# Optimization experiments

Measured on AMD Instinct MI355X. Metric: run time of the kernel, lower is better.

The kernel has to match this reference:

```python
import jax, jax.numpy as jnp
import numpy as np

B, S, VOCAB, HID, NCLS = 64, 512, 1400, 256, 128


def _time_lstm(W_all, b_all, U_all, b_u, W_d, b_d, x, ts):
    # x: [b, s, h], ts: [b, s]
    b = x.shape[0]
    h0 = jnp.zeros((b, HID), x.dtype)
    c0 = jnp.zeros((b, HID), x.dtype)

    def step(carry, xt):
        h, c = carry
        x_t, t_t = xt  # [b,h], [b]
        c_s1 = jnp.tanh(c @ W_d.T + b_d)
        c_adj = (c - c_s1) + c_s1 * t_t[:, None]
        gates = jax.nn.sigmoid(h @ W_all.T + b_all + x_t @ U_all.T + b_u)
        f, i, o, c_tmp = jnp.split(gates, 4, axis=1)  # note: c_tmp is sigmoid, as in source
        c_new = f * c_adj + i * c_tmp
        h_new = o * jnp.tanh(c_new)
        return (h_new, c_new), h_new

    _, hs = jax.lax.scan(step, (h0, c0), (x.transpose(1, 0, 2), ts.T))
    return hs.transpose(1, 0, 2)  # [b, s, h]


def setup_inputs() -> dict:
    key = jax.random.key(0)
    ks = jax.random.split(key, 18)

    def g(k, shape, scale=0.05):
        return jax.random.normal(k, shape, dtype=jnp.float32) * scale

    return {
        "inputs": jax.random.uniform(ks[0], (B, S, VOCAB), dtype=jnp.float32),
        "timestamps": jax.random.uniform(ks[1], (B, S), dtype=jnp.float32),
        "emb": g(ks[2], (VOCAB, HID)),
        "W_all1": g(ks[3], (4 * HID, HID)), "b_all1": g(ks[4], (4 * HID,)),
        "U_all1": g(ks[5], (4 * HID, HID)), "b_u1": g(ks[6], (4 * HID,)),
        "W_d1": g(ks[7], (HID, HID)), "b_d1": g(ks[8], (HID,)),
        "W_all2": g(ks[9], (4 * HID, HID)), "b_all2": g(ks[10], (4 * HID,)),
        "U_all2": g(ks[11], (4 * HID, HID)), "b_u2": g(ks[12], (4 * HID,)),
        "W_d2": g(ks[13], (HID, HID)), "b_d2": g(ks[14], (HID,)),
        "wa": g(ks[15], (1, HID)),
        "Wb": g(ks[16], (HID, HID)),
        "W_out": g(ks[17], (NCLS, HID)),
    }


def reference(inputs, timestamps, emb, W_all1, b_all1, U_all1, b_u1, W_d1, b_d1,
              W_all2, b_all2, U_all2, b_u2, W_d2, b_d2, wa, Wb, W_out):
    embedded = jnp.einsum('bsv,vh->bsh', inputs, emb)  # multi-hot embedding lookup
    out1 = _time_lstm(W_all1, b_all1, U_all1, b_u1, W_d1, b_d1, embedded, timestamps)
    out2 = _time_lstm(W_all2, b_all2, U_all2, b_u2, W_d2, b_d2, embedded, timestamps)
    alpha = jax.nn.softmax(jnp.einsum('bsh,oh->bs', out1, wa), axis=1)  # [b,s]
    Beta = jnp.tanh(jnp.einsum('bsh,gh->bsg', out2, Wb))  # [b,s,h]
    ctx = jnp.sum(embedded * Beta * alpha[:, :, None], axis=1)  # [b,h]
    return ctx @ W_out.T  # [b, num_classes]
```

## Files before the change

kernel.cpp:

```cpp
#include <hip/hip_runtime.h>

typedef __attribute__((ext_vector_type(8))) short short8;
typedef __attribute__((ext_vector_type(4))) float f32x4;

#define B_   64
#define S_   512
#define V_   1400
#define VP_  1408
#define H_   256
#define G4_  1024
#define NC_  128
#define CH_  64

__device__ __forceinline__ unsigned short f2bf(float f) {
    unsigned u = __builtin_bit_cast(unsigned, f);
    u += 0x7FFFu + ((u >> 16) & 1u);
    return (unsigned short)(u >> 16);
}
__device__ __forceinline__ float bf2f(unsigned short h) {
    unsigned u = ((unsigned)h) << 16;
    return __builtin_bit_cast(float, u);
}
__device__ __forceinline__ float fsig(float x) {
    x = fminf(fmaxf(x, -40.f), 40.f);
    float e = __builtin_amdgcn_exp2f(x * -1.44269504f);
    return __builtin_amdgcn_rcpf(1.0f + e);
}
__device__ __forceinline__ float ftanh(float x) {
    x = fminf(fmaxf(x, -40.f), 40.f);
    float e = __builtin_amdgcn_exp2f(x * 2.88539008f);
    return 1.0f - 2.0f * __builtin_amdgcn_rcpf(e + 1.0f);
}

__device__ __forceinline__ short8 gload16_sc1(const unsigned short* p) {
    short8 r;
    asm volatile("global_load_dwordx4 %0, %1, off sc1"
                 : "=&v"(r) : "v"((unsigned long long)p));
    return r;
}
__device__ __forceinline__ void gstore_short_sc1(unsigned short* p, unsigned v) {
    asm volatile("global_store_short %0, %1, off sc1"
                 :: "v"((unsigned long long)p), "v"(v));
}
__device__ __forceinline__ float gloadf_plain(const float* p) {
    float r;
    asm volatile("global_load_dword %0, %1, off"
                 : "=&v"(r) : "v"((unsigned long long)p));
    return r;
}

#define CNT_ZONE_ 4096

__global__ void k0_prep(const float* __restrict__ emb,
                        const float* __restrict__ Wa1, const float* __restrict__ Wa2,
                        const float* __restrict__ Wd1, const float* __restrict__ Wd2,
                        const float* __restrict__ U1,  const float* __restrict__ U2,
                        const float* __restrict__ ba1, const float* __restrict__ bu1,
                        const float* __restrict__ ba2, const float* __restrict__ bu2,
                        const float* __restrict__ Wb,
                        unsigned short* __restrict__ embT, unsigned short* __restrict__ Wg,
                        unsigned short* __restrict__ Wd,   unsigned short* __restrict__ Ub,
                        unsigned short* __restrict__ Wbb,  float* __restrict__ bg,
                        unsigned int* __restrict__ cnt) {
    int tid = blockIdx.x * blockDim.x + threadIdx.x;
    int np = gridDim.x * blockDim.x;
    for (int i = tid; i < 256 * VP_; i += np) {
        int n = i / VP_, k = i - n * VP_;
        embT[i] = (k < V_) ? f2bf(emb[k * H_ + n]) : (unsigned short)0;
    }
    for (int i = tid; i < G4_ * H_; i += np) {
        Wg[i] = f2bf(Wa1[i]); Wg[G4_ * H_ + i] = f2bf(Wa2[i]);
        Ub[i] = f2bf(U1[i]);  Ub[G4_ * H_ + i] = f2bf(U2[i]);
    }
    for (int i = tid; i < H_ * H_; i += np) {
        Wd[i] = f2bf(Wd1[i]); Wd[H_ * H_ + i] = f2bf(Wd2[i]); Wbb[i] = f2bf(Wb[i]);
    }
    for (int i = tid; i < G4_; i += np) {
        bg[i] = ba1[i] + bu1[i]; bg[G4_ + i] = ba2[i] + bu2[i];
    }
    for (int i = tid; i < CNT_ZONE_; i += np) cnt[i] = 0;
}

__global__ __launch_bounds__(512, 2) void k1_embed(const float* __restrict__ inputs,
                                                   const unsigned short* __restrict__ embT,
                                                   unsigned short* __restrict__ embB) {
    const int tid = threadIdx.x;
    const int w = tid >> 6, ln = tid & 63, q = ln >> 4, l16 = ln & 15;
    const int mt = w >> 2, ng = (w & 3) * 4;
    const int Rbase = blockIdx.x * 32 + mt * 16;
    const float* arow = inputs + (long)(Rbase + l16) * V_;

    f32x4 acc[4];
    #pragma unroll
    for (int i = 0; i < 4; ++i) acc[i] = (f32x4){0.f, 0.f, 0.f, 0.f};

    for (int kt = 0; kt < 44; ++kt) {
        int k0 = kt * 32 + q * 8;
        short8 af;
        if (kt == 43 && q == 3) {
            #pragma unroll
            for (int j = 0; j < 8; ++j) af[j] = 0;
        } else {
            f32x4 x0 = *(const f32x4*)(arow + k0);
            f32x4 x1 = *(const f32x4*)(arow + k0 + 4);
            #pragma unroll
            for (int j = 0; j < 4; ++j) { af[j] = (short)f2bf(x0[j]); af[4 + j] = (short)f2bf(x1[j]); }
        }
        #pragma unroll
        for (int i = 0; i < 4; ++i) {
            short8 bf = *(const short8*)(embT + (long)((ng + i) * 16 + l16) * VP_ + k0);
            acc[i] = __builtin_amdgcn_mfma_f32_16x16x32_bf16(af, bf, acc[i], 0, 0, 0);
        }
    }
    #pragma unroll
    for (int i = 0; i < 4; ++i) {
        int col = (ng + i) * 16 + l16;
        #pragma unroll
        for (int j = 0; j < 4; ++j) {
            int R = Rbase + 4 * q + j;
            embB[(long)R * H_ + col] = f2bf(acc[i][j]);
        }
    }
}

__global__ __launch_bounds__(512, 2) void k2_pre(const unsigned short* __restrict__ embB,
                                                 const unsigned short* __restrict__ Ub,
                                                 const float* __restrict__ bg,
                                                 float* __restrict__ P, int t0) {
    const int tid = threadIdx.x;
    const int w = tid >> 6, ln = tid & 63, q = ln >> 4, l16 = ln & 15;
    const int rbase = blockIdx.x * 32;

    short8 af[2][8];
    #pragma unroll
    for (int mt = 0; mt < 2; ++mt)
        #pragma unroll
        for (int kt = 0; kt < 8; ++kt) {
            int rp = rbase + mt * 16 + l16;
            int rg = t0 * 64 + rp;
            int b = rg & 63, s = rg >> 6;
            af[mt][kt] = *(const short8*)(embB + ((long)b * S_ + s) * H_ + kt * 32 + q * 8);
        }

    for (int i = 0; i < 16; ++i) {
        int nt2 = w * 16 + i;
        int l = nt2 >> 6;
        int gcol = (nt2 & 63) * 16 + l16;
        float bias = bg[nt2 * 16 + l16];
        short8 bf[8];
        #pragma unroll
        for (int kt = 0; kt < 8; ++kt)
            bf[kt] = *(const short8*)(Ub + (long)(nt2 * 16 + l16) * H_ + kt * 32 + q * 8);
        #pragma unroll
        for (int mt = 0; mt < 2; ++mt) {
            f32x4 acc = (f32x4){bias, bias, bias, bias};
            #pragma unroll
            for (int kt = 0; kt < 8; ++kt)
                acc = __builtin_amdgcn_mfma_f32_16x16x32_bf16(af[mt][kt], bf[kt], acc, 0, 0, 0);
            int rp0 = rbase + mt * 16;
            float* dst = P + ((long)l * (CH_ * 64) + rp0 + 4 * q) * G4_ + gcol;
            #pragma unroll
            for (int j = 0; j < 4; ++j) dst[(long)j * G4_] = acc[j];
        }
    }
}

__global__ __launch_bounds__(256, 1) void k3_fused(const float* __restrict__ ts,
                                                   const unsigned short* __restrict__ W,
                                                   const float* __restrict__ bd1,
                                                   const float* __restrict__ bd2,
                                                   const float* __restrict__ Pcur,
                                                   unsigned short* __restrict__ out1,
                                                   unsigned short* __restrict__ out2,
                                                   float* __restrict__ cst,
                                                   unsigned short* __restrict__ cx,
                                                   unsigned int* __restrict__ cnt,
                                                   int t0,
                                                   const unsigned short* __restrict__ embB,
                                                   const unsigned short* __restrict__ Ub,
                                                   const float* __restrict__ bg,
                                                   float* __restrict__ Pnext,
                                                   int next_t0) {
    const int tid = threadIdx.x;
    const int w = tid >> 6, ln = tid & 63, q = ln >> 4, l16 = ln & 15;
    const int bid = blockIdx.x;

    if (bid >= 32) {
        const int g2 = bid - 32;
        const int rbase = (g2 >> 1) * 32;
        const int hb = g2 & 1;

        short8 af[2][8];
        #pragma unroll
        for (int mt = 0; mt < 2; ++mt)
            #pragma unroll
            for (int kt = 0; kt < 8; ++kt) {
                int rp = rbase + mt * 16 + l16;
                int rg = next_t0 * 64 + rp;
                int b = rg & 63, s = rg >> 6;
                af[mt][kt] = *(const short8*)(embB + ((long)b * S_ + s) * H_ + kt * 32 + q * 8);
            }

        for (int i = 0; i < 16; ++i) {
            int nt2 = hb * 64 + w * 16 + i;
            int l = nt2 >> 6;
            int gcol = (nt2 & 63) * 16 + l16;
            float bias = bg[nt2 * 16 + l16];
            short8 bf[8];
            #pragma unroll
            for (int kt = 0; kt < 8; ++kt)
                bf[kt] = *(const short8*)(Ub + (long)(nt2 * 16 + l16) * H_ + kt * 32 + q * 8);
            #pragma unroll
            for (int mt = 0; mt < 2; ++mt) {
                f32x4 acc = (f32x4){bias, bias, bias, bias};
                #pragma unroll
                for (int kt = 0; kt < 8; ++kt)
                    acc = __builtin_amdgcn_mfma_f32_16x16x32_bf16(af[mt][kt], bf[kt], acc, 0, 0, 0);
                int rp0 = rbase + mt * 16;
                float* dst = Pnext + ((long)l * (CH_ * 64) + rp0 + 4 * q) * G4_ + gcol;
                #pragma unroll
                for (int j = 0; j < 4; ++j) dst[(long)j * G4_] = acc[j];
            }
        }
        return;
    }

    __shared__ float ts_lds[16][CH_];

    const int chunk = t0 >> 6;
    const int grp = bid & 7, cg = bid >> 3;
    const int l = grp >> 2, m = grp & 3, b0 = m * 16;
    const int hc0 = cg * 64 + w * 16;
    const int mycol = hc0 + l16;
    unsigned int* cell = cnt + (chunk * 8 + grp) * 64;
    unsigned short* outp = l ? out2 : out1;
    const float bdv = (l ? bd2 : bd1)[mycol];

    for (int i = tid; i < 16 * CH_; i += 256) {
        int r = i >> 6, cc = i & (CH_ - 1);
        ts_lds[r][cc] = ts[(b0 + r) * S_ + t0 + cc];
    }

    short8 wg[4][8];
    short8 wd[8];
    #pragma unroll
    for (int g = 0; g < 4; ++g)
        #pragma unroll
        for (int kt = 0; kt < 8; ++kt)
            wg[g][kt] = *(const short8*)(W + ((long)(l * G4_ + g * H_ + mycol)) * H_ + kt * 32 + q * 8);
    #pragma unroll
    for (int kt = 0; kt < 8; ++kt)
        wd[kt] = *(const short8*)(W + (long)2 * G4_ * H_ + ((long)(l * H_ + mycol)) * H_ + kt * 32 + q * 8);

    float cf[4];
    if (t0 == 0) {
        cf[0] = cf[1] = cf[2] = cf[3] = 0.f;
    } else {
        #pragma unroll
        for (int j = 0; j < 4; ++j)
            cf[j] = cst[(long)grp * 4096 + (4 * q + j) * 256 + mycol];
    }
    __syncthreads();

    const float* Pbase = Pcur + ((long)l * (CH_ * 64) + b0) * G4_;
    unsigned opaque_zero;
    asm volatile("v_mov_b32 %0, 0" : "=v"(opaque_zero));

    #pragma unroll 1
    for (int t = 0; t < CH_; ++t) {
        const int gt = t0 + t;

        if (t) {
            if (tid == 0) {
                const unsigned tgt = 4u * (unsigned)t;
                unsigned it = 0;
                for (;;) {
                    unsigned v = __hip_atomic_fetch_add(cell, opaque_zero,
                                                        __ATOMIC_RELAXED, __HIP_MEMORY_SCOPE_AGENT);
                    if (v >= tgt || ++it >= (1u << 15)) break;
                }
            }
            __syncthreads();
        }
        __builtin_amdgcn_sched_barrier(0);

        short8 ha[8], ca[8];
        if (gt == 0) {
            #pragma unroll
            for (int kt = 0; kt < 8; ++kt) {
                #pragma unroll
                for (int jj = 0; jj < 8; ++jj) { ha[kt][jj] = 0; ca[kt][jj] = 0; }
            }
        } else {
            const unsigned short* crow = cx + ((long)(((gt - 1) & 1) * 8 + grp)) * 4096 + l16 * 256 + q * 8;
            const unsigned short* hrow = outp + ((long)(b0 + l16) * S_ + (gt - 1)) * H_ + q * 8;
            #pragma unroll
            for (int kt = 0; kt < 8; ++kt) ca[kt] = gload16_sc1(crow + kt * 32);
            #pragma unroll
            for (int kt = 0; kt < 8; ++kt) ha[kt] = gload16_sc1(hrow + kt * 32);
        }
        float pv[4][4];
        #pragma unroll
        for (int g = 0; g < 4; ++g)
            #pragma unroll
            for (int j = 0; j < 4; ++j)
                pv[g][j] = gloadf_plain(Pbase + ((long)t * 64 + 4 * q + j) * G4_ + g * H_ + mycol);

        asm volatile("s_waitcnt vmcnt(24)" ::: "memory");
        __builtin_amdgcn_sched_barrier(0);
        f32x4 dacc = (f32x4){bdv, bdv, bdv, bdv};
        #pragma unroll
        for (int kt = 0; kt < 8; ++kt)
            dacc = __builtin_amdgcn_mfma_f32_16x16x32_bf16(ca[kt], wd[kt], dacc, 0, 0, 0);

        asm volatile("s_waitcnt vmcnt(16)" ::: "memory");
        __builtin_amdgcn_sched_barrier(0);
        f32x4 gacc[4];
        #pragma unroll
        for (int g = 0; g < 4; ++g) {
            gacc[g] = (f32x4){0.f, 0.f, 0.f, 0.f};
            #pragma unroll
            for (int kt = 0; kt < 8; ++kt)
                gacc[g] = __builtin_amdgcn_mfma_f32_16x16x32_bf16(ha[kt], wg[g][kt], gacc[g], 0, 0, 0);
        }

        asm volatile("s_waitcnt vmcnt(0)" ::: "memory");
        __builtin_amdgcn_sched_barrier(0);

        #pragma unroll
        for (int j = 0; j < 4; ++j) {
            int r = 4 * q + j;
            float tv = ts_lds[r][t];
            float cs1 = ftanh(dacc[j]);
            float cadj = cf[j] + cs1 * (tv - 1.0f);
            float fg = fsig(gacc[0][j] + pv[0][j]);
            float ig = fsig(gacc[1][j] + pv[1][j]);
            float og = fsig(gacc[2][j] + pv[2][j]);
            float cg2 = fsig(gacc[3][j] + pv[3][j]);
            float cn = fg * cadj + ig * cg2;
            float hn = og * ftanh(cn);
            cf[j] = cn;
            gstore_short_sc1(outp + ((long)(b0 + r) * S_ + gt) * H_ + mycol, (unsigned)f2bf(hn));
            gstore_short_sc1(cx + ((long)((gt & 1) * 8 + grp)) * 4096 + r * 256 + mycol, (unsigned)f2bf(cn));
        }

        asm volatile("s_waitcnt vmcnt(0)" ::: "memory");
        __syncthreads();
        if (tid == 0)
            (void)__hip_atomic_fetch_add(cell, 1u, __ATOMIC_RELAXED, __HIP_MEMORY_SCOPE_AGENT);
    }

    #pragma unroll
    for (int j = 0; j < 4; ++j)
        cst[(long)grp * 4096 + (4 * q + j) * 256 + mycol] = cf[j];
}

__global__ __launch_bounds__(512, 2) void k4_all(const unsigned short* __restrict__ out1,
                                                 const unsigned short* __restrict__ out2,
                                                 const unsigned short* __restrict__ Wbb,
                                                 const unsigned short* __restrict__ embB,
                                                 const float* __restrict__ wa,
                                                 const float* __restrict__ Wout,
                                                 float* __restrict__ out) {
    __shared__ float sc[512];
    __shared__ float red[512];
    __shared__ float alp_l[512];
    __shared__ float cbuf[32][256];
    __shared__ float ctx_l[256];
    const int b = blockIdx.x, tid = threadIdx.x;
    const int w = tid >> 6, ln = tid & 63, q = ln >> 4, l16 = ln & 15;

    f32x4 wv = *(const f32x4*)(wa + ln * 4);
    for (int i = 0; i < 64; ++i) {
        int s = w * 64 + i;
        const unsigned short* row = out1 + ((long)b * S_ + s) * H_ + ln * 4;
        float d = bf2f(row[0]) * wv[0] + bf2f(row[1]) * wv[1] +
                  bf2f(row[2]) * wv[2] + bf2f(row[3]) * wv[3];
        #pragma unroll
        for (int off = 32; off; off >>= 1) d += __shfl_xor(d, off);
        if (ln == 0) sc[s] = d;
    }
    __syncthreads();
    float v = sc[tid];
    red[tid] = v;
    for (int st = 256; st; st >>= 1) {
        __syncthreads();
        if (tid < st) red[tid] = fmaxf(red[tid], red[tid + st]);
    }
    __syncthreads();
    float M = red[0];
    __syncthreads();
    float e = __builtin_amdgcn_exp2f((v - M) * 1.44269504f);
    red[tid] = e;
    for (int st = 256; st; st >>= 1) {
        __syncthreads();
        if (tid < st) red[tid] += red[tid + st];
    }
    __syncthreads();
    alp_l[tid] = e * __builtin_amdgcn_rcpf(red[0]);
    __syncthreads();

    float cp[16];
    #pragma unroll
    for (int nt = 0; nt < 16; ++nt) cp[nt] = 0.f;

    for (int i = 0; i < 4; ++i) {
        int mt = w * 4 + i;
        short8 af[8];
        #pragma unroll
        for (int kt = 0; kt < 8; ++kt)
            af[kt] = *(const short8*)(out2 + ((long)b * S_ + mt * 16 + l16) * H_ + kt * 32 + q * 8);
        float al[4];
        #pragma unroll
        for (int j = 0; j < 4; ++j) al[j] = alp_l[mt * 16 + 4 * q + j];
        for (int nt = 0; nt < 16; ++nt) {
            f32x4 acc = (f32x4){0.f, 0.f, 0.f, 0.f};
            #pragma unroll
            for (int kt = 0; kt < 8; ++kt) {
                short8 bf = *(const short8*)(Wbb + (long)(nt * 16 + l16) * H_ + kt * 32 + q * 8);
                acc = __builtin_amdgcn_mfma_f32_16x16x32_bf16(af[kt], bf, acc, 0, 0, 0);
            }
            #pragma unroll
            for (int j = 0; j < 4; ++j) {
                int s = mt * 16 + 4 * q + j;
                float beta = ftanh(acc[j]);
                float ev = bf2f(embB[((long)b * S_ + s) * H_ + nt * 16 + l16]);
                cp[nt] += beta * al[j] * ev;
            }
        }
    }
    #pragma unroll
    for (int nt = 0; nt < 16; ++nt) cbuf[w * 4 + q][nt * 16 + l16] = cp[nt];
    __syncthreads();
    if (tid < 256) {
        float sum = 0.f;
        for (int i = 0; i < 32; ++i) sum += cbuf[i][tid];
        ctx_l[tid] = sum;
    }
    __syncthreads();

    if (tid < NC_) {
        const float* cr = ctx_l;
        const f32x4* wr = (const f32x4*)(Wout + tid * H_);
        float acc = 0.f;
        #pragma unroll 8
        for (int i = 0; i < 64; ++i) {
            f32x4 ww = wr[i];
            acc += cr[4 * i] * ww[0] + cr[4 * i + 1] * ww[1] +
                   cr[4 * i + 2] * ww[2] + cr[4 * i + 3] * ww[3];
        }
        out[b * NC_ + tid] = acc;
    }
}

extern "C" void kernel_launch(void* const* d_in, const int* in_sizes, int n_in,
                              void* d_out, int out_size, void* d_ws, size_t ws_size,
                              hipStream_t stream) {
    (void)in_sizes; (void)n_in; (void)out_size;
    const float* inputs = (const float*)d_in[0];
    const float* tsp    = (const float*)d_in[1];
    const float* emb    = (const float*)d_in[2];
    const float* Wa1 = (const float*)d_in[3];  const float* ba1 = (const float*)d_in[4];
    const float* U1  = (const float*)d_in[5];  const float* bu1 = (const float*)d_in[6];
    const float* Wd1 = (const float*)d_in[7];  const float* bd1 = (const float*)d_in[8];
    const float* Wa2 = (const float*)d_in[9];  const float* ba2 = (const float*)d_in[10];
    const float* U2  = (const float*)d_in[11]; const float* bu2 = (const float*)d_in[12];
    const float* Wd2 = (const float*)d_in[13]; const float* bd2 = (const float*)d_in[14];
    const float* wa  = (const float*)d_in[15];
    const float* Wb  = (const float*)d_in[16];
    const float* Wout = (const float*)d_in[17];
    float* out = (float*)d_out;

    char* ws = (char*)d_ws;
    unsigned short* embT = (unsigned short*)(ws + 0);
    unsigned short* Wg   = (unsigned short*)(ws + 720896);
    unsigned short* Wd   = (unsigned short*)(ws + 1769472);
    unsigned short* Ub   = (unsigned short*)(ws + 2031616);
    unsigned short* Wbb  = (unsigned short*)(ws + 3080192);
    float*          bgp  = (float*)(ws + 3211264);
    unsigned short* embB = (unsigned short*)(ws + 3219456);
    float*          P0   = (float*)(ws + 19996672);
    unsigned short* out1 = (unsigned short*)(ws + 53551104);
    unsigned short* out2 = (unsigned short*)(ws + 70328320);
    unsigned short* cx   = (unsigned short*)(ws + 87105536);
    float*          cst  = (float*)(ws + 87236608);
    unsigned int*   cnt  = (unsigned int*)(ws + 87564288);
    float*          P1   = (float*)(ws + 87719936);
    const size_t NEED_FUSED = 121274368;
    const bool fuse = (ws_size >= NEED_FUSED);

    hipLaunchKernelGGL(k0_prep, dim3(256), dim3(256), 0, stream,
                       emb, Wa1, Wa2, Wd1, Wd2, U1, U2, ba1, bu1, ba2, bu2, Wb,
                       embT, Wg, Wd, Ub, Wbb, bgp, cnt);
    hipLaunchKernelGGL(k1_embed, dim3(1024), dim3(512), 0, stream, inputs, embT, embB);
    hipLaunchKernelGGL(k2_pre, dim3(128), dim3(512), 0, stream, embB, Ub, bgp, P0, 0);

    float* Pb[2] = { P0, fuse ? P1 : P0 };
    for (int c = 0; c < 8; ++c) {
        if (fuse) {
            int ng = (c < 7) ? 256 : 0;
            hipLaunchKernelGGL(k3_fused, dim3(32 + ng), dim3(256), 0, stream,
                               tsp, Wg, bd1, bd2, Pb[c & 1], out1, out2, cst, cx, cnt, c * CH_,
                               embB, Ub, bgp, Pb[(c + 1) & 1], (c + 1) * CH_);
        } else {
            if (c > 0)
                hipLaunchKernelGGL(k2_pre, dim3(128), dim3(512), 0, stream, embB, Ub, bgp, P0, c * CH_);
            hipLaunchKernelGGL(k3_fused, dim3(32), dim3(256), 0, stream,
                               tsp, Wg, bd1, bd2, P0, out1, out2, cst, cx, cnt, c * CH_,
                               embB, Ub, bgp, P0, S_ );
        }
    }
    hipLaunchKernelGGL(k4_all, dim3(64), dim3(512), 0, stream,
                       out1, out2, Wbb, embB, wa, Wout, out);
}
```

Measured before the change: 2.833 ms.

## Replace counter barrier with tagged h/c exchange words polled per step

Drops the per-step atomic counter plus block barrier between the recurrent blocks. Each h and c value is now published as a 32-bit word with the timestep in the high half, and consumers spin-load those words until every tag matches. The aim is to cut the serialized barrier and atomic round-trip latency out of the 512-step recurrence. In exchange it writes twice as many bytes to the exchange buffers and adds polling loads and checks, and it relies on the visibility of sc1 stores.

```diff
diff --git a/kernel.cpp b/kernel.cpp
--- a/kernel.cpp
+++ b/kernel.cpp
@@ -2,6 +2,7 @@
 
 typedef __attribute__((ext_vector_type(8))) short short8;
 typedef __attribute__((ext_vector_type(4))) float f32x4;
+typedef __attribute__((ext_vector_type(4))) unsigned int u32x4;
 
 #define B_   64
 #define S_   512
@@ -32,14 +33,18 @@
     return 1.0f - 2.0f * __builtin_amdgcn_rcpf(e + 1.0f);
 }
 
-__device__ __forceinline__ short8 gload16_sc1(const unsigned short* p) {
-    short8 r;
+__device__ __forceinline__ u32x4 gload16u_sc1(const unsigned int* p) {
+    u32x4 r;
     asm volatile("global_load_dwordx4 %0, %1, off sc1"
                  : "=&v"(r) : "v"((unsigned long long)p));
     return r;
 }
-__device__ __forceinline__ void gstore_short_sc1(unsigned short* p, unsigned v) {
-    asm volatile("global_store_short %0, %1, off sc1"
+__device__ __forceinline__ void gstore_dword_sc1(unsigned int* p, unsigned v) {
+    asm volatile("global_store_dword %0, %1, off sc1"
+                 :: "v"((unsigned long long)p), "v"(v));
+}
+__device__ __forceinline__ void gstore_short_plain(unsigned short* p, unsigned v) {
+    asm volatile("global_store_short %0, %1, off"
                  :: "v"((unsigned long long)p), "v"(v));
 }
 __device__ __forceinline__ float gloadf_plain(const float* p) {
@@ -49,7 +54,7 @@
     return r;
 }
 
-#define CNT_ZONE_ 4096
+#define XW_WORDS_ (2 * 8 * 16 * 256)
 
 __global__ void k0_prep(const float* __restrict__ emb,
                         const float* __restrict__ Wa1, const float* __restrict__ Wa2,
@@ -61,7 +66,7 @@
                         unsigned short* __restrict__ embT, unsigned short* __restrict__ Wg,
                         unsigned short* __restrict__ Wd,   unsigned short* __restrict__ Ub,
                         unsigned short* __restrict__ Wbb,  float* __restrict__ bg,
-                        unsigned int* __restrict__ cnt) {
+                        unsigned int* __restrict__ hxw, unsigned int* __restrict__ cxw) {
     int tid = blockIdx.x * blockDim.x + threadIdx.x;
     int np = gridDim.x * blockDim.x;
     for (int i = tid; i < 256 * VP_; i += np) {
@@ -78,7 +83,7 @@
     for (int i = tid; i < G4_; i += np) {
         bg[i] = ba1[i] + bu1[i]; bg[G4_ + i] = ba2[i] + bu2[i];
     }
-    for (int i = tid; i < CNT_ZONE_; i += np) cnt[i] = 0;
+    for (int i = tid; i < XW_WORDS_; i += np) { hxw[i] = 0; cxw[i] = 0; }
 }
 
 __global__ __launch_bounds__(512, 2) void k1_embed(const float* __restrict__ inputs,
@@ -173,8 +178,8 @@
                                                    unsigned short* __restrict__ out1,
                                                    unsigned short* __restrict__ out2,
                                                    float* __restrict__ cst,
-                                                   unsigned short* __restrict__ cx,
-                                                   unsigned int* __restrict__ cnt,
+                                                   unsigned int* __restrict__ hxw,
+                                                   unsigned int* __restrict__ cxw,
                                                    int t0,
                                                    const unsigned short* __restrict__ embB,
                                                    const unsigned short* __restrict__ Ub,
@@ -227,12 +232,10 @@
 
     __shared__ float ts_lds[16][CH_];
 
-    const int chunk = t0 >> 6;
     const int grp = bid & 7, cg = bid >> 3;
     const int l = grp >> 2, m = grp & 3, b0 = m * 16;
     const int hc0 = cg * 64 + w * 16;
     const int mycol = hc0 + l16;
-    unsigned int* cell = cnt + (chunk * 8 + grp) * 64;
     unsigned short* outp = l ? out2 : out1;
     const float bdv = (l ? bd2 : bd1)[mycol];
 
@@ -263,58 +266,122 @@
     __syncthreads();
 
     const float* Pbase = Pcur + ((long)l * (CH_ * 64) + b0) * G4_;
-    unsigned opaque_zero;
-    asm volatile("v_mov_b32 %0, 0" : "=v"(opaque_zero));
 
     #pragma unroll 1
     for (int t = 0; t < CH_; ++t) {
         const int gt = t0 + t;
 
-        if (t) {
-            if (tid == 0) {
-                const unsigned tgt = 4u * (unsigned)t;
+        short8 ha[8], ca[8];
+        f32x4 dacc = (f32x4){bdv, bdv, bdv, bdv};
+        float pv[4][4];
+
+        if (gt == 0) {
+            #pragma unroll
+            for (int kt = 0; kt < 8; ++kt) {
+                #pragma unroll
+                for (int jj = 0; jj < 8; ++jj) { ha[kt][jj] = 0; ca[kt][jj] = 0; }
+            }
+            #pragma unroll
+            for (int g = 0; g < 4; ++g)
+                #pragma unroll
+                for (int j = 0; j < 4; ++j)
+                    pv[g][j] = gloadf_plain(Pbase + ((long)t * 64 + 4 * q + j) * G4_ + g * H_ + mycol);
+            asm volatile("s_waitcnt vmcnt(0)" ::: "memory");
+            __builtin_amdgcn_sched_barrier(0);
+        } else {
+            const unsigned slotR = (unsigned)((gt - 1) & 1);
+            const unsigned int* cbase = cxw + ((slotR * 8 + grp) * 16 + l16) * 256 + q * 8;
+            const unsigned int* hbase = hxw + ((slotR * 8 + grp) * 16 + l16) * 256 + q * 8;
+            const unsigned expw = (unsigned)gt << 16;
+
+            {
+                u32x4 cw[16];
                 unsigned it = 0;
                 for (;;) {
-                    unsigned v = __hip_atomic_fetch_add(cell, opaque_zero,
-                                                        __ATOMIC_RELAXED, __HIP_MEMORY_SCOPE_AGENT);
-                    if (v >= tgt || ++it >= (1u << 15)) break;
+                    #pragma unroll
+                    for (int kt = 0; kt < 8; ++kt) {
+                        cw[2 * kt]     = gload16u_sc1(cbase + kt * 32);
+                        cw[2 * kt + 1] = gload16u_sc1(cbase + kt * 32 + 4);
+                    }
+                    asm volatile("s_waitcnt vmcnt(0)" ::: "memory");
+                    __builtin_amdgcn_sched_barrier(0);
+                    unsigned bad = 0;
+                    #pragma unroll
+                    for (int i = 0; i < 16; ++i)
+                        #pragma unroll
+                        for (int j2 = 0; j2 < 4; ++j2)
+                            bad |= (cw[i][j2] ^ expw) & 0xFFFF0000u;
+                    if (__all(bad == 0) || ++it >= 64u) break;
                 }
-            }
-            __syncthreads();
-        }
-        __builtin_amdgcn_sched_barrier(0);
-
-        short8 ha[8], ca[8];
-        if (gt == 0) {
+                #pragma unroll
+                for (int kt = 0; kt < 8; ++kt) {
+                    short8 cv;
+                    #pragma unroll
+                    for (int j2 = 0; j2 < 4; ++j2) {
+                        cv[j2]     = (short)cw[2 * kt][j2];
+                        cv[4 + j2] = (short)cw[2 * kt + 1][j2];
+                    }
+                    ca[kt] = cv;
+                }
+            }
+
+            u32x4 hw[16];
             #pragma unroll
             for (int kt = 0; kt < 8; ++kt) {
-                #pragma unroll
-                for (int jj = 0; jj < 8; ++jj) { ha[kt][jj] = 0; ca[kt][jj] = 0; }
-            }
-        } else {
-            const unsigned short* crow = cx + ((long)(((gt - 1) & 1) * 8 + grp)) * 4096 + l16 * 256 + q * 8;
-            const unsigned short* hrow = outp + ((long)(b0 + l16) * S_ + (gt - 1)) * H_ + q * 8;
-            #pragma unroll
-            for (int kt = 0; kt < 8; ++kt) ca[kt] = gload16_sc1(crow + kt * 32);
-            #pragma unroll
-            for (int kt = 0; kt < 8; ++kt) ha[kt] = gload16_sc1(hrow + kt * 32);
-        }
-        float pv[4][4];
-        #pragma unroll
-        for (int g = 0; g < 4; ++g)
-            #pragma unroll
-            for (int j = 0; j < 4; ++j)
-                pv[g][j] = gloadf_plain(Pbase + ((long)t * 64 + 4 * q + j) * G4_ + g * H_ + mycol);
-
-        asm volatile("s_waitcnt vmcnt(24)" ::: "memory");
-        __builtin_amdgcn_sched_barrier(0);
-        f32x4 dacc = (f32x4){bdv, bdv, bdv, bdv};
-        #pragma unroll
-        for (int kt = 0; kt < 8; ++kt)
-            dacc = __builtin_amdgcn_mfma_f32_16x16x32_bf16(ca[kt], wd[kt], dacc, 0, 0, 0);
-
-        asm volatile("s_waitcnt vmcnt(16)" ::: "memory");
-        __builtin_amdgcn_sched_barrier(0);
+                hw[2 * kt]     = gload16u_sc1(hbase + kt * 32);
+                hw[2 * kt + 1] = gload16u_sc1(hbase + kt * 32 + 4);
+            }
+            #pragma unroll
+            for (int g = 0; g < 4; ++g)
+                #pragma unroll
+                for (int j = 0; j < 4; ++j)
+                    pv[g][j] = gloadf_plain(Pbase + ((long)t * 64 + 4 * q + j) * G4_ + g * H_ + mycol);
+
+            #pragma unroll
+            for (int kt = 0; kt < 8; ++kt)
+                dacc = __builtin_amdgcn_mfma_f32_16x16x32_bf16(ca[kt], wd[kt], dacc, 0, 0, 0);
+
+            asm volatile("s_waitcnt vmcnt(16)" ::: "memory");
+            __builtin_amdgcn_sched_barrier(0);
+            {
+                unsigned bad = 0;
+                #pragma unroll
+                for (int i = 0; i < 16; ++i)
+                    #pragma unroll
+                    for (int j2 = 0; j2 < 4; ++j2)
+                        bad |= (hw[i][j2] ^ expw) & 0xFFFF0000u;
+                if (!__all(bad == 0)) {
+                    unsigned it = 0;
+                    for (;;) {
+                        #pragma unroll
+                        for (int kt = 0; kt < 8; ++kt) {
+                            hw[2 * kt]     = gload16u_sc1(hbase + kt * 32);
+                            hw[2 * kt + 1] = gload16u_sc1(hbase + kt * 32 + 4);
+                        }
+                        asm volatile("s_waitcnt vmcnt(0)" ::: "memory");
+                        __builtin_amdgcn_sched_barrier(0);
+                        unsigned bad2 = 0;
+                        #pragma unroll
+                        for (int i = 0; i < 16; ++i)
+                            #pragma unroll
+                            for (int j2 = 0; j2 < 4; ++j2)
+                                bad2 |= (hw[i][j2] ^ expw) & 0xFFFF0000u;
+                        if (__all(bad2 == 0) || ++it >= 64u) break;
+                    }
+                }
+            }
+            #pragma unroll
+            for (int kt = 0; kt < 8; ++kt) {
+                short8 hv;
+                #pragma unroll
+                for (int j2 = 0; j2 < 4; ++j2) {
+                    hv[j2]     = (short)hw[2 * kt][j2];
+                    hv[4 + j2] = (short)hw[2 * kt + 1][j2];
+                }
+                ha[kt] = hv;
+            }
+        }
+
         f32x4 gacc[4];
         #pragma unroll
         for (int g = 0; g < 4; ++g) {
@@ -323,10 +390,19 @@
             for (int kt = 0; kt < 8; ++kt)
                 gacc[g] = __builtin_amdgcn_mfma_f32_16x16x32_bf16(ha[kt], wg[g][kt], gacc[g], 0, 0, 0);
         }
+        if (gt == 0) {
+            #pragma unroll
+            for (int kt = 0; kt < 8; ++kt)
+                dacc = __builtin_amdgcn_mfma_f32_16x16x32_bf16(ca[kt], wd[kt], dacc, 0, 0, 0);
+        }
 
         asm volatile("s_waitcnt vmcnt(0)" ::: "memory");
         __builtin_amdgcn_sched_barrier(0);
 
+        const unsigned tagw = ((unsigned)(gt + 1)) << 16;
+        const unsigned wslot = (unsigned)(gt & 1);
+        unsigned int* cdst = cxw + ((wslot * 8 + grp) * 16) * 256 + mycol;
+        unsigned int* hdst = hxw + ((wslot * 8 + grp) * 16) * 256 + mycol;
         #pragma unroll
         for (int j = 0; j < 4; ++j) {
             int r = 4 * q + j;
@@ -340,14 +416,11 @@
             float cn = fg * cadj + ig * cg2;
             float hn = og * ftanh(cn);
             cf[j] = cn;
-            gstore_short_sc1(outp + ((long)(b0 + r) * S_ + gt) * H_ + mycol, (unsigned)f2bf(hn));
-            gstore_short_sc1(cx + ((long)((gt & 1) * 8 + grp)) * 4096 + r * 256 + mycol, (unsigned)f2bf(cn));
-        }
-
-        asm volatile("s_waitcnt vmcnt(0)" ::: "memory");
-        __syncthreads();
-        if (tid == 0)
-            (void)__hip_atomic_fetch_add(cell, 1u, __ATOMIC_RELAXED, __HIP_MEMORY_SCOPE_AGENT);
+            unsigned short hb = f2bf(hn), cb = f2bf(cn);
+            gstore_short_plain(outp + ((long)(b0 + r) * S_ + gt) * H_ + mycol, (unsigned)hb);
+            gstore_dword_sc1(hdst + r * 256, tagw | (unsigned)hb);
+            gstore_dword_sc1(cdst + r * 256, tagw | (unsigned)cb);
+        }
     }
 
     #pragma unroll
@@ -482,16 +555,16 @@
     float*          P0   = (float*)(ws + 19996672);
     unsigned short* out1 = (unsigned short*)(ws + 53551104);
     unsigned short* out2 = (unsigned short*)(ws + 70328320);
-    unsigned short* cx   = (unsigned short*)(ws + 87105536);
-    float*          cst  = (float*)(ws + 87236608);
-    unsigned int*   cnt  = (unsigned int*)(ws + 87564288);
-    float*          P1   = (float*)(ws + 87719936);
-    const size_t NEED_FUSED = 121274368;
+    float*          cst  = (float*)(ws + 87105536);
+    unsigned int*   hxw  = (unsigned int*)(ws + 87236608);
+    unsigned int*   cxw  = (unsigned int*)(ws + 87498752);
+    float*          P1   = (float*)(ws + 87760896);
+    const size_t NEED_FUSED = 121315328;
     const bool fuse = (ws_size >= NEED_FUSED);
 
     hipLaunchKernelGGL(k0_prep, dim3(256), dim3(256), 0, stream,
                        emb, Wa1, Wa2, Wd1, Wd2, U1, U2, ba1, bu1, ba2, bu2, Wb,
-                       embT, Wg, Wd, Ub, Wbb, bgp, cnt);
+                       embT, Wg, Wd, Ub, Wbb, bgp, hxw, cxw);
     hipLaunchKernelGGL(k1_embed, dim3(1024), dim3(512), 0, stream, inputs, embT, embB);
     hipLaunchKernelGGL(k2_pre, dim3(128), dim3(512), 0, stream, embB, Ub, bgp, P0, 0);
 
@@ -500,13 +573,13 @@
         if (fuse) {
             int ng = (c < 7) ? 256 : 0;
             hipLaunchKernelGGL(k3_fused, dim3(32 + ng), dim3(256), 0, stream,
-                               tsp, Wg, bd1, bd2, Pb[c & 1], out1, out2, cst, cx, cnt, c * CH_,
+                               tsp, Wg, bd1, bd2, Pb[c & 1], out1, out2, cst, hxw, cxw, c * CH_,
                                embB, Ub, bgp, Pb[(c + 1) & 1], (c + 1) * CH_);
         } else {
             if (c > 0)
                 hipLaunchKernelGGL(k2_pre, dim3(128), dim3(512), 0, stream, embB, Ub, bgp, P0, c * CH_);
             hipLaunchKernelGGL(k3_fused, dim3(32), dim3(256), 0, stream,
-                               tsp, Wg, bd1, bd2, P0, out1, out2, cst, cx, cnt, c * CH_,
+                               tsp, Wg, bd1, bd2, P0, out1, out2, cst, hxw, cxw, c * CH_,
                                embB, Ub, bgp, P0, S_ );
         }
     }
```

After: 4.660 ms. 64.5% more time.
